# Kernel optimization log

Hardware: AMD Instinct MI355X
Metric: run time of the kernel (lower is better)

## Reference

```python
import jax, jax.numpy as jnp
import numpy as np

T, B, D_IN, D_HID, D_OUT = 512, 64, 512, 512, 512


def setup_inputs() -> dict:
    key = jax.random.key(0)
    k_x, k_xh, k_hh, k_o = jax.random.split(key, 4)
    return {
        "x": jax.random.normal(k_x, (T, B, D_IN), dtype=jnp.float32),
        "xh": jax.random.normal(k_xh, (D_IN, D_HID), dtype=jnp.float32) * 0.01,
        "hh": jax.random.normal(k_hh, (D_HID, D_HID), dtype=jnp.float32) * 0.01,
        "hb": jnp.zeros((D_HID,), dtype=jnp.float32),
        "o": jax.random.normal(k_o, (D_HID, D_OUT), dtype=jnp.float32) * 0.01,
        "h0": jnp.zeros((1, D_HID), dtype=jnp.float32),
    }


def reference(x, xh, hh, hb, o, h0):
    # Elman RNN (training branch): h_t = relu(x_t @ xh + h_{t-1} @ hh + hb); y_t = h_t @ o
    # h starts as (1, hid) and broadcasts to (B, hid) at step 1, as in the torch code.
    batch = x.shape[1]
    h_init = jnp.broadcast_to(h0, (batch, h0.shape[1]))

    def step(h, xi):  # xi: [B, D_IN], h: [B, D_HID]
        h = jax.nn.relu(xi @ xh + h @ hh + hb)
        return h, h @ o  # y: [B, D_OUT]

    _, ys = jax.lax.scan(step, h_init, x)
    return ys  # [T, B, D_OUT] (stacked version of the torch list of outputs)
```

## Files before the change

### kernel.cpp

```cpp
#include <hip/hip_runtime.h>
#include <hip/hip_bf16.h>

#define TSTEPS 512
#define BATCH  64
#define DIM    512
#define NWG    8

using short8 = __attribute__((ext_vector_type(8))) short;
using f32x4  = __attribute__((ext_vector_type(4))) float;

__device__ __forceinline__ unsigned short f2bf(float f) {
    unsigned u = __builtin_bit_cast(unsigned, f);
    unsigned r = (u + 0x7FFFu + ((u >> 16) & 1u)) >> 16;
    return (unsigned short)r;
}

__global__ void conv_T(const float* __restrict__ src, unsigned short* __restrict__ dst) {
    __shared__ float tile[32][33];
    const int bx = blockIdx.x * 32, by = blockIdx.y * 32;
    const int tx = threadIdx.x & 31, ty = threadIdx.x >> 5;
#pragma unroll
    for (int k = 0; k < 32; k += 8)
        tile[ty + k][tx] = src[(size_t)(by + ty + k) * DIM + bx + tx];
    __syncthreads();
#pragma unroll
    for (int k = 0; k < 32; k += 8)
        dst[(size_t)(bx + ty + k) * DIM + by + tx] = f2bf(tile[tx][ty + k]);
}

__global__ __launch_bounds__(256) void gemm_xwm(
    const float* __restrict__ X,
    const unsigned short* __restrict__ Bt,
    const float* __restrict__ bias, float* __restrict__ Out)
{
    __shared__ unsigned short As[128 * 40];
    __shared__ unsigned short Bs[128 * 40];
    const int tid = threadIdx.x;
    const int m0 = blockIdx.x * 128, n0 = blockIdx.y * 128;
    const int lane = tid & 63, wv = tid >> 6;
    const int ln15 = lane & 15, kg = lane >> 4;
    const int wr = (wv >> 1) * 64, wc = (wv & 1) * 64;

    f32x4 acc[4][4];
#pragma unroll
    for (int m = 0; m < 4; ++m)
#pragma unroll
        for (int n = 0; n < 4; ++n) acc[m][n] = f32x4{0.f, 0.f, 0.f, 0.f};

    const int arow = tid >> 1, ahalf = tid & 1;
    for (int k0 = 0; k0 < DIM; k0 += 32) {
        const float4* ga = reinterpret_cast<const float4*>(
            X + (size_t)(m0 + arow) * DIM + k0 + ahalf * 16);
        float4 a0 = ga[0], a1 = ga[1], a2 = ga[2], a3 = ga[3];
        const ulonglong2* gb = reinterpret_cast<const ulonglong2*>(
            Bt + (size_t)(n0 + arow) * DIM + k0 + ahalf * 16);
        ulonglong2 bv0 = gb[0], bv1 = gb[1];
        __syncthreads();
        {
            unsigned long long p[4];
            const float4 av[4] = {a0, a1, a2, a3};
#pragma unroll
            for (int q = 0; q < 4; ++q)
                p[q] = (unsigned long long)f2bf(av[q].x)
                     | ((unsigned long long)f2bf(av[q].y) << 16)
                     | ((unsigned long long)f2bf(av[q].z) << 32)
                     | ((unsigned long long)f2bf(av[q].w) << 48);
            unsigned long long* s = reinterpret_cast<unsigned long long*>(&As[arow * 40 + ahalf * 16]);
            s[0] = p[0]; s[1] = p[1]; s[2] = p[2]; s[3] = p[3];
            *reinterpret_cast<ulonglong2*>(&Bs[arow * 40 + ahalf * 16]) = bv0;
            *reinterpret_cast<ulonglong2*>(&Bs[arow * 40 + ahalf * 16 + 8]) = bv1;
        }
        __syncthreads();
        short8 af[4], bf[4];
#pragma unroll
        for (int m = 0; m < 4; ++m)
            af[m] = *reinterpret_cast<const short8*>(&As[(wr + m * 16 + ln15) * 40 + kg * 8]);
#pragma unroll
        for (int n = 0; n < 4; ++n)
            bf[n] = *reinterpret_cast<const short8*>(&Bs[(wc + n * 16 + ln15) * 40 + kg * 8]);
#pragma unroll
        for (int m = 0; m < 4; ++m)
#pragma unroll
            for (int n = 0; n < 4; ++n)
                acc[m][n] = __builtin_amdgcn_mfma_f32_16x16x32_bf16(af[m], bf[n], acc[m][n], 0, 0, 0);
    }
    float4* Out4 = reinterpret_cast<float4*>(Out);
#pragma unroll
    for (int n = 0; n < 4; ++n) {
        int col = n0 + wc + n * 16 + ln15;
        float bb = bias[col];
#pragma unroll
        for (int m = 0; m < 4; ++m) {
            int t = (m0 + wr) >> 6;
            float4 v;
            v.x = acc[m][n][0] + bb; v.y = acc[m][n][1] + bb;
            v.z = acc[m][n][2] + bb; v.w = acc[m][n][3] + bb;
            Out4[(((size_t)t * 4 + kg) * 4 + m) * DIM + col] = v;
        }
    }
}

__global__ __launch_bounds__(256, 1) void rnn_scan(
    const float* __restrict__ hh, const float* __restrict__ xwb,
    const float* __restrict__ h0, unsigned long long* __restrict__ tbuf,
    unsigned short* __restrict__ hist)
{
    const int tid  = threadIdx.x;
    const int wg   = blockIdx.x;
    const int lane = tid & 63;
    const int wv   = __builtin_amdgcn_readfirstlane(tid >> 6);
    const int ln15 = lane & 15, kg = lane >> 4;
    const int colw = wg * 64 + wv * 16 + ln15;

    __shared__ unsigned long long hsU[2 * 8192];

    short8 Bhh[16];
#pragma unroll
    for (int kk = 0; kk < 16; ++kk) {
        short8 bh;
#pragma unroll
        for (int j = 0; j < 8; ++j) {
            int k = kk * 32 + kg * 8 + j;
            bh[j] = (short)f2bf(hh[(size_t)k * DIM + colw]);
        }
        Bhh[kk] = bh;
    }

    {
        int colp = wg * 32 + (tid & 31);
        unsigned pair = (unsigned)f2bf(h0[2 * colp]) | ((unsigned)f2bf(h0[2 * colp + 1]) << 16);
        unsigned long long v = (unsigned long long)pair | (1ull << 32);
#pragma unroll
        for (int q = 0; q < 8; ++q) {
            int row = (tid >> 5) * 8 + q;
            __hip_atomic_store(&tbuf[row * 256 + colp], v,
                               __ATOMIC_RELAXED, __HIP_MEMORY_SCOPE_AGENT);
        }
    }

    const float4* xw4 = reinterpret_cast<const float4*>(xwb);

    for (int t = 0; t < TSTEPS; ++t) {
        f32x4 xwr[4];
#pragma unroll
        for (int m = 0; m < 4; ++m) {
            float4 v = xw4[(((size_t)t * 4 + kg) * 4 + m) * DIM + colw];
            xwr[m] = f32x4{v.x, v.y, v.z, v.w};
        }

        const unsigned long long* src = tbuf + (size_t)(t % 3) * 16384 + tid;
        const unsigned expect = (unsigned)(t + 1);
        char* lbase = reinterpret_cast<char*>(hsU) + (t & 1) * 65536;
#pragma unroll 1
        for (int half = 0; half < 2; ++half) {
            unsigned long long va[32];
            for (;;) {
#pragma unroll
                for (int a = 0; a < 32; ++a)
                    va[a] = __hip_atomic_load(src + (half * 32 + a) * 256,
                                              __ATOMIC_RELAXED, __HIP_MEMORY_SCOPE_AGENT);
                unsigned acc = 0;
#pragma unroll
                for (int a = 0; a < 32; ++a)
                    acc |= ((unsigned)(va[a] >> 32)) ^ expect;
                if (!__any((acc & 0xffffu) != 0)) break;
                __builtin_amdgcn_s_sleep(1);
            }
#pragma unroll
            for (int a = 0; a < 32; ++a) {
                int row = half * 32 + a;
                int byte = ((row << 10) + (tid << 2)) ^ ((row & 7) << 4);
                *reinterpret_cast<unsigned*>(lbase + byte) = (unsigned)va[a];
            }
        }
        __syncthreads();

        f32x4 acch[4];
#pragma unroll
        for (int m = 0; m < 4; ++m) acch[m] = f32x4{0.f, 0.f, 0.f, 0.f};
#pragma unroll
        for (int kk = 0; kk < 16; ++kk) {
#pragma unroll
            for (int m = 0; m < 4; ++m) {
                int row = m * 16 + ln15;
                int byte = ((row << 10) + (kk << 6) + (kg << 4)) ^ ((row & 7) << 4);
                short8 a = *reinterpret_cast<const short8*>(lbase + byte);
                acch[m] = __builtin_amdgcn_mfma_f32_16x16x32_bf16(a, Bhh[kk], acch[m], 0, 0, 0);
            }
        }

        const unsigned long long tagbits = ((unsigned long long)(t + 2)) << 32;
        unsigned long long* tdst = tbuf + (size_t)((t + 1) % 3) * 16384;
        unsigned short* hdst = hist + (size_t)(t + 1) * (BATCH * DIM);
        const bool evenlane = (ln15 & 1) == 0;
        const int colp = colw >> 1;
#pragma unroll
        for (int m = 0; m < 4; ++m)
#pragma unroll
            for (int r = 0; r < 4; ++r) {
                int row = m * 16 + kg * 4 + r;
                float hn = xwr[m][r] + acch[m][r];
                hn = hn > 0.f ? hn : 0.f;
                unsigned self = f2bf(hn);
                hdst[(size_t)row * DIM + colw] = (unsigned short)self;
                unsigned partner = (unsigned)__shfl_xor((int)self, 1);
                unsigned pair = evenlane ? (self | (partner << 16))
                                         : (partner | (self << 16));
                if (evenlane == (m < 2))
                    __hip_atomic_store(&tdst[row * 256 + colp], tagbits | (unsigned long long)pair,
                                       __ATOMIC_RELAXED, __HIP_MEMORY_SCOPE_AGENT);
            }
    }
}

__global__ __launch_bounds__(256) void gemm_y(
    const unsigned short* __restrict__ A,
    const unsigned short* __restrict__ Bt,
    float* __restrict__ Out)
{
    __shared__ unsigned short As[128 * 40];
    __shared__ unsigned short Bs[128 * 40];
    const int tid = threadIdx.x;
    const int m0 = blockIdx.x * 128, n0 = blockIdx.y * 128;
    const int lane = tid & 63, wv = tid >> 6;
    const int ln15 = lane & 15, kg = lane >> 4;
    const int wr = (wv >> 1) * 64, wc = (wv & 1) * 64;

    f32x4 acc[4][4];
#pragma unroll
    for (int m = 0; m < 4; ++m)
#pragma unroll
        for (int n = 0; n < 4; ++n) acc[m][n] = f32x4{0.f, 0.f, 0.f, 0.f};

    const int sr = tid & 127;
    for (int k0 = 0; k0 < DIM; k0 += 32) {
        const unsigned short* g = (tid < 128)
            ? A  + (size_t)(m0 + sr) * DIM + k0
            : Bt + (size_t)(n0 + sr) * DIM + k0;
        unsigned short* s = (tid < 128) ? &As[sr * 40] : &Bs[sr * 40];
        ulonglong2 v0 = reinterpret_cast<const ulonglong2*>(g)[0];
        ulonglong2 v1 = reinterpret_cast<const ulonglong2*>(g)[1];
        ulonglong2 v2 = reinterpret_cast<const ulonglong2*>(g)[2];
        ulonglong2 v3 = reinterpret_cast<const ulonglong2*>(g)[3];
        __syncthreads();
        reinterpret_cast<ulonglong2*>(s)[0] = v0;
        reinterpret_cast<ulonglong2*>(s)[1] = v1;
        reinterpret_cast<ulonglong2*>(s)[2] = v2;
        reinterpret_cast<ulonglong2*>(s)[3] = v3;
        __syncthreads();
        short8 af[4], bf[4];
#pragma unroll
        for (int m = 0; m < 4; ++m)
            af[m] = *reinterpret_cast<const short8*>(&As[(wr + m * 16 + ln15) * 40 + kg * 8]);
#pragma unroll
        for (int n = 0; n < 4; ++n)
            bf[n] = *reinterpret_cast<const short8*>(&Bs[(wc + n * 16 + ln15) * 40 + kg * 8]);
#pragma unroll
        for (int m = 0; m < 4; ++m)
#pragma unroll
            for (int n = 0; n < 4; ++n)
                acc[m][n] = __builtin_amdgcn_mfma_f32_16x16x32_bf16(af[m], bf[n], acc[m][n], 0, 0, 0);
    }
#pragma unroll
    for (int m = 0; m < 4; ++m)
#pragma unroll
        for (int n = 0; n < 4; ++n)
#pragma unroll
            for (int r = 0; r < 4; ++r) {
                int row = m0 + wr + m * 16 + kg * 4 + r;
                int col = n0 + wc + n * 16 + ln15;
                Out[(size_t)row * DIM + col] = acc[m][n][r];
            }
}

extern "C" void kernel_launch(void* const* d_in, const int* in_sizes, int n_in,
                              void* d_out, int out_size, void* d_ws, size_t ws_size,
                              hipStream_t stream) {
    const float* x  = (const float*)d_in[0];
    const float* xh = (const float*)d_in[1];
    const float* hh = (const float*)d_in[2];
    const float* hb = (const float*)d_in[3];
    const float* o  = (const float*)d_in[4];
    const float* h0 = (const float*)d_in[5];
    float* out = (float*)d_out;

    unsigned long long* tbuf = (unsigned long long*)d_ws;
    unsigned short* hist = (unsigned short*)((char*)d_ws + 393216);
    unsigned short* oT  = (unsigned short*)((char*)d_ws + 393216 + (size_t)513 * 65536);
    unsigned short* xhT = oT + (size_t)DIM * DIM;

    (void)hipMemsetAsync(d_ws, 0, 393216, stream);
    conv_T<<<dim3(16, 16), 256, 0, stream>>>(o, oT);
    conv_T<<<dim3(16, 16), 256, 0, stream>>>(xh, xhT);
    gemm_xwm<<<dim3(256, 4), 256, 0, stream>>>(x, xhT, hb, out);
    rnn_scan<<<NWG, 256, 0, stream>>>(hh, out, h0, tbuf, hist);
    gemm_y<<<dim3(256, 4), 256, 0, stream>>>(hist + 32768, oT, out);
}
```

Before: 2.487 ms.

## Replace tagged exchange buffer with per-wave flags and direct history reads in RNN scan

```diff
diff --git a/kernel.cpp b/kernel.cpp
--- a/kernel.cpp
+++ b/kernel.cpp
@@ -95,121 +95,131 @@
             float4 v;
             v.x = acc[m][n][0] + bb; v.y = acc[m][n][1] + bb;
             v.z = acc[m][n][2] + bb; v.w = acc[m][n][3] + bb;
-            Out4[(((size_t)t * 4 + kg) * 4 + m) * DIM + col] = v;
+            Out4[(((size_t)t * 4 + m) * 4 + kg) * DIM + col] = v;
         }
     }
 }
 
 __global__ __launch_bounds__(256, 1) void rnn_scan(
     const float* __restrict__ hh, const float* __restrict__ xwb,
-    const float* __restrict__ h0, unsigned long long* __restrict__ tbuf,
-    unsigned short* __restrict__ hist)
+    const float* __restrict__ h0, unsigned short* hist,
+    unsigned int* flags)
 {
     const int tid  = threadIdx.x;
     const int wg   = blockIdx.x;
     const int lane = tid & 63;
     const int wv   = __builtin_amdgcn_readfirstlane(tid >> 6);
     const int ln15 = lane & 15, kg = lane >> 4;
-    const int colw = wg * 64 + wv * 16 + ln15;
-
-    __shared__ unsigned long long hsU[2 * 8192];
-
-    short8 Bhh[16];
-#pragma unroll
-    for (int kk = 0; kk < 16; ++kk) {
-        short8 bh;
-#pragma unroll
-        for (int j = 0; j < 8; ++j) {
-            int k = kk * 32 + kg * 8 + j;
-            bh[j] = (short)f2bf(hh[(size_t)k * DIM + colw]);
-        }
-        Bhh[kk] = bh;
+    const bool even = (ln15 & 1) == 0;
+
+    short8 Bhh[4][16];
+#pragma unroll
+    for (int n = 0; n < 4; ++n) {
+        const int col = wg * 64 + n * 16 + ln15;
+#pragma unroll
+        for (int kk = 0; kk < 16; ++kk) {
+            short8 b;
+#pragma unroll
+            for (int j = 0; j < 8; ++j)
+                b[j] = (short)f2bf(hh[(size_t)(kk * 32 + kg * 8 + j) * DIM + col]);
+            Bhh[n][kk] = b;
+        }
     }
 
     {
-        int colp = wg * 32 + (tid & 31);
-        unsigned pair = (unsigned)f2bf(h0[2 * colp]) | ((unsigned)f2bf(h0[2 * colp + 1]) << 16);
-        unsigned long long v = (unsigned long long)pair | (1ull << 32);
-#pragma unroll
-        for (int q = 0; q < 8; ++q) {
-            int row = (tid >> 5) * 8 + q;
-            __hip_atomic_store(&tbuf[row * 256 + colp], v,
-                               __ATOMIC_RELAXED, __HIP_MEMORY_SCOPE_AGENT);
-        }
-    }
+        unsigned* hd32 = reinterpret_cast<unsigned*>(hist);
+#pragma unroll
+        for (int n = 0; n < 4; ++n) {
+            int col = wg * 64 + n * 16 + ln15;
+            unsigned self = f2bf(h0[col]);
+            unsigned partner = (unsigned)__shfl_xor((int)self, 1);
+            unsigned pair = even ? (self | (partner << 16)) : (partner | (self << 16));
+            if (even == (n < 2)) {
+                int colp = col >> 1;
+#pragma unroll
+                for (int r = 0; r < 4; ++r) {
+                    int row = 16 * wv + kg * 4 + r;
+                    __hip_atomic_store(&hd32[row * 256 + colp], pair,
+                                       __ATOMIC_RELAXED, __HIP_MEMORY_SCOPE_AGENT);
+                }
+            }
+        }
+    }
+    asm volatile("s_waitcnt vmcnt(0)" ::: "memory");
+    if (lane == 0)
+        __hip_atomic_store(&flags[wg * 4 + wv], 1u, __ATOMIC_RELAXED, __HIP_MEMORY_SCOPE_AGENT);
 
     const float4* xw4 = reinterpret_cast<const float4*>(xwb);
+    typedef union { unsigned long long u[2]; short8 s; } cvt8;
 
     for (int t = 0; t < TSTEPS; ++t) {
-        f32x4 xwr[4];
-#pragma unroll
-        for (int m = 0; m < 4; ++m) {
-            float4 v = xw4[(((size_t)t * 4 + kg) * 4 + m) * DIM + colw];
-            xwr[m] = f32x4{v.x, v.y, v.z, v.w};
-        }
-
-        const unsigned long long* src = tbuf + (size_t)(t % 3) * 16384 + tid;
+        f32x4 xw_[4];
+#pragma unroll
+        for (int n = 0; n < 4; ++n) {
+            float4 v = xw4[(((size_t)t * 4 + wv) * 4 + kg) * DIM + wg * 64 + n * 16 + ln15];
+            xw_[n] = f32x4{v.x, v.y, v.z, v.w};
+        }
+
+        f32x4 acc[4];
+#pragma unroll
+        for (int n = 0; n < 4; ++n) acc[n] = f32x4{0.f, 0.f, 0.f, 0.f};
+
+        const unsigned long long* hrow = reinterpret_cast<const unsigned long long*>(
+            hist + (size_t)t * (BATCH * DIM) + (size_t)(16 * wv + ln15) * DIM);
         const unsigned expect = (unsigned)(t + 1);
-        char* lbase = reinterpret_cast<char*>(hsU) + (t & 1) * 65536;
-#pragma unroll 1
-        for (int half = 0; half < 2; ++half) {
-            unsigned long long va[32];
-            for (;;) {
-#pragma unroll
-                for (int a = 0; a < 32; ++a)
-                    va[a] = __hip_atomic_load(src + (half * 32 + a) * 256,
-                                              __ATOMIC_RELAXED, __HIP_MEMORY_SCOPE_AGENT);
-                unsigned acc = 0;
-#pragma unroll
-                for (int a = 0; a < 32; ++a)
-                    acc |= ((unsigned)(va[a] >> 32)) ^ expect;
-                if (!__any((acc & 0xffffu) != 0)) break;
-                __builtin_amdgcn_s_sleep(1);
+
+        unsigned done = 0;
+        while (done != 0xffu) {
+            unsigned fl = __hip_atomic_load(&flags[(lane & 7) * 4 + wv],
+                                            __ATOMIC_RELAXED, __HIP_MEMORY_SCOPE_AGENT);
+            unsigned long long bal = __ballot(fl >= expect);
+            unsigned ready = ((unsigned)bal & 0xffu) & ~done;
+            if (ready == 0) { __builtin_amdgcn_s_sleep(1); continue; }
+#pragma unroll
+            for (int j = 0; j < 8; ++j) {
+                if (ready & (1u << j)) {
+                    cvt8 a0, a1;
+                    a0.u[0] = __hip_atomic_load(hrow + (2 * j) * 8 + kg * 2,
+                                                __ATOMIC_RELAXED, __HIP_MEMORY_SCOPE_AGENT);
+                    a0.u[1] = __hip_atomic_load(hrow + (2 * j) * 8 + kg * 2 + 1,
+                                                __ATOMIC_RELAXED, __HIP_MEMORY_SCOPE_AGENT);
+                    a1.u[0] = __hip_atomic_load(hrow + (2 * j + 1) * 8 + kg * 2,
+                                                __ATOMIC_RELAXED, __HIP_MEMORY_SCOPE_AGENT);
+                    a1.u[1] = __hip_atomic_load(hrow + (2 * j + 1) * 8 + kg * 2 + 1,
+                                                __ATOMIC_RELAXED, __HIP_MEMORY_SCOPE_AGENT);
+#pragma unroll
+                    for (int n = 0; n < 4; ++n) {
+                        acc[n] = __builtin_amdgcn_mfma_f32_16x16x32_bf16(a0.s, Bhh[n][2 * j],     acc[n], 0, 0, 0);
+                        acc[n] = __builtin_amdgcn_mfma_f32_16x16x32_bf16(a1.s, Bhh[n][2 * j + 1], acc[n], 0, 0, 0);
+                    }
+                }
             }
-#pragma unroll
-            for (int a = 0; a < 32; ++a) {
-                int row = half * 32 + a;
-                int byte = ((row << 10) + (tid << 2)) ^ ((row & 7) << 4);
-                *reinterpret_cast<unsigned*>(lbase + byte) = (unsigned)va[a];
-            }
-        }
-        __syncthreads();
-
-        f32x4 acch[4];
-#pragma unroll
-        for (int m = 0; m < 4; ++m) acch[m] = f32x4{0.f, 0.f, 0.f, 0.f};
-#pragma unroll
-        for (int kk = 0; kk < 16; ++kk) {
-#pragma unroll
-            for (int m = 0; m < 4; ++m) {
-                int row = m * 16 + ln15;
-                int byte = ((row << 10) + (kk << 6) + (kg << 4)) ^ ((row & 7) << 4);
-                short8 a = *reinterpret_cast<const short8*>(lbase + byte);
-                acch[m] = __builtin_amdgcn_mfma_f32_16x16x32_bf16(a, Bhh[kk], acch[m], 0, 0, 0);
-            }
-        }
-
-        const unsigned long long tagbits = ((unsigned long long)(t + 2)) << 32;
-        unsigned long long* tdst = tbuf + (size_t)((t + 1) % 3) * 16384;
-        unsigned short* hdst = hist + (size_t)(t + 1) * (BATCH * DIM);
-        const bool evenlane = (ln15 & 1) == 0;
-        const int colp = colw >> 1;
-#pragma unroll
-        for (int m = 0; m < 4; ++m)
+            done |= ready;
+        }
+
+        unsigned* hd32 = reinterpret_cast<unsigned*>(hist + (size_t)(t + 1) * (BATCH * DIM));
+#pragma unroll
+        for (int n = 0; n < 4; ++n) {
+            int col = wg * 64 + n * 16 + ln15;
+            int colp = col >> 1;
 #pragma unroll
             for (int r = 0; r < 4; ++r) {
-                int row = m * 16 + kg * 4 + r;
-                float hn = xwr[m][r] + acch[m][r];
+                float hn = xw_[n][r] + acc[n][r];
                 hn = hn > 0.f ? hn : 0.f;
                 unsigned self = f2bf(hn);
-                hdst[(size_t)row * DIM + colw] = (unsigned short)self;
                 unsigned partner = (unsigned)__shfl_xor((int)self, 1);
-                unsigned pair = evenlane ? (self | (partner << 16))
-                                         : (partner | (self << 16));
-                if (evenlane == (m < 2))
-                    __hip_atomic_store(&tdst[row * 256 + colp], tagbits | (unsigned long long)pair,
+                unsigned pair = even ? (self | (partner << 16)) : (partner | (self << 16));
+                if (even == (n < 2)) {
+                    int row = 16 * wv + kg * 4 + r;
+                    __hip_atomic_store(&hd32[row * 256 + colp], pair,
                                        __ATOMIC_RELAXED, __HIP_MEMORY_SCOPE_AGENT);
+                }
             }
+        }
+        asm volatile("s_waitcnt vmcnt(0)" ::: "memory");
+        if (lane == 0)
+            __hip_atomic_store(&flags[wg * 4 + wv], (unsigned)(t + 2),
+                               __ATOMIC_RELAXED, __HIP_MEMORY_SCOPE_AGENT);
     }
 }
 
@@ -284,15 +294,15 @@
     const float* h0 = (const float*)d_in[5];
     float* out = (float*)d_out;
 
-    unsigned long long* tbuf = (unsigned long long*)d_ws;
-    unsigned short* hist = (unsigned short*)((char*)d_ws + 393216);
-    unsigned short* oT  = (unsigned short*)((char*)d_ws + 393216 + (size_t)513 * 65536);
+    unsigned int* flags = (unsigned int*)d_ws;
+    unsigned short* hist = (unsigned short*)((char*)d_ws + 4096);
+    unsigned short* oT  = (unsigned short*)((char*)d_ws + 4096 + (size_t)513 * 65536);
     unsigned short* xhT = oT + (size_t)DIM * DIM;
 
-    (void)hipMemsetAsync(d_ws, 0, 393216, stream);
+    (void)hipMemsetAsync(d_ws, 0, 4096, stream);
     conv_T<<<dim3(16, 16), 256, 0, stream>>>(o, oT);
     conv_T<<<dim3(16, 16), 256, 0, stream>>>(xh, xhT);
     gemm_xwm<<<dim3(256, 4), 256, 0, stream>>>(x, xhT, hb, out);
-    rnn_scan<<<NWG, 256, 0, stream>>>(hh, out, h0, tbuf, hist);
+    rnn_scan<<<NWG, 256, 0, stream>>>(hh, out, h0, hist, flags);
     gemm_y<<<dim3(256, 4), 256, 0, stream>>>(hist + 32768, oT, out);
 }
```

Result: slower. 3.632 ms (+46.0%).
